# Kernel tuning notes

Hardware: AMD Instinct MI355X
Metric: run time of the kernel (lower is better)

Reference implementation:

```python
import jax, jax.numpy as jnp
import numpy as np


def setup_inputs() -> dict:
    key = jax.random.key(0)
    k1, k2, k3 = jax.random.split(key, 3)
    shape = (2, 16, 2048, 64)  # (b, num_heads, seq_len, d_k)
    Q = jax.random.normal(k1, shape, dtype=jnp.float32)
    K = jax.random.normal(k2, shape, dtype=jnp.float32)
    V = jax.random.normal(k3, shape, dtype=jnp.float32)
    return {"Q": Q, "K": K, "V": V}


def reference(Q, K, V):
    # Mathematically identical to the blockwise online-softmax loop:
    # causal softmax attention with scale 1/sqrt(d_k), plus logsumexp L.
    d_k = Q.shape[-1]
    seq_len = Q.shape[2]
    scale = 1.0 / np.sqrt(d_k).astype(np.float32)
    # scores: [b, h, q, k]
    S = jnp.einsum("bhqd,bhkd->bhqk", Q, K) * scale
    causal_mask = jnp.tril(jnp.ones((seq_len, seq_len), dtype=bool))  # k_pos <= q_pos
    S = jnp.where(causal_mask, S, -jnp.inf)
    # L_i = m_i + log(l_i) == logsumexp over key dim (every row has >=1 valid key)
    L = jax.nn.logsumexp(S, axis=-1, keepdims=True)  # [b, h, q, 1]
    P = jnp.exp(S - L)  # normalized probabilities (deferred-normalization result)
    O = jnp.einsum("bhqk,bhkd->bhqd", P, V)
    return O, L
```

## Files before the change

kernel.cpp:

```cpp
#include <hip/hip_runtime.h>
#include <hip/hip_bf16.h>

#define S_LEN 2048
#define DH    64
#define NBH   32
#define KSCALE 0.1803368801111f
#define LN2    0.6931471805599453f
#define MB2    4.0f

typedef short v4s __attribute__((ext_vector_type(4)));
typedef short v8s __attribute__((ext_vector_type(8)));
typedef float v4f __attribute__((ext_vector_type(4)));

__device__ __forceinline__ unsigned short f2bf(float f){
  union { float f; unsigned int u; } v; v.f = f;
  return (unsigned short)((v.u + 0x7FFFu + ((v.u >> 16) & 1u)) >> 16);
}

__device__ __forceinline__ void gld16(void* lds, const void* g){
  __builtin_amdgcn_global_load_lds(
      (const __attribute__((address_space(1))) unsigned int*)g,
      (__attribute__((address_space(3))) unsigned int*)lds, 16, 0, 0);
}

__global__ __launch_bounds__(256) void prep(const float* __restrict__ K,
                                            const float* __restrict__ V,
                                            unsigned short* __restrict__ Kf,
                                            unsigned short* __restrict__ Vf){
  __shared__ unsigned short s[64 * 72];
  const int t   = blockIdx.x;
  const int bh  = blockIdx.y;
  const int tid = threadIdx.x;

  const float* Ksrc = K + ((size_t)bh * S_LEN + t * 64) * DH;
  #pragma unroll
  for (int i = 0; i < 4; ++i){
    int f = tid + i * 256;
    float4 v = ((const float4*)Ksrc)[f];
    int row = f >> 4, col = (f & 15) * 4;
    ushort4 o; o.x = f2bf(v.x); o.y = f2bf(v.y); o.z = f2bf(v.z); o.w = f2bf(v.w);
    *(ushort4*)(&s[row * 72 + col]) = o;
  }
  __syncthreads();
  unsigned short* KfT = Kf + ((size_t)bh * 32 + t) * 4096;
  #pragma unroll
  for (int i = 0; i < 2; ++i){
    int item = tid + i * 256;
    int c = item >> 6, l = item & 63;
    int kb = c >> 1, h = c & 1;
    v8s frag = *(const v8s*)(&s[(kb * 16 + (l & 15)) * 72 + h * 32 + (l >> 4) * 8]);
    *(v8s*)(&KfT[c * 512 + l * 8]) = frag;
  }
  __syncthreads();

  const float* Vsrc = V + ((size_t)bh * S_LEN + t * 64) * DH;
  #pragma unroll
  for (int i = 0; i < 4; ++i){
    int f = tid + i * 256;
    float4 v = ((const float4*)Vsrc)[f];
    int k = f >> 4, d = (f & 15) * 4;
    s[(d + 0) * 72 + k] = f2bf(v.x);
    s[(d + 1) * 72 + k] = f2bf(v.y);
    s[(d + 2) * 72 + k] = f2bf(v.z);
    s[(d + 3) * 72 + k] = f2bf(v.w);
  }
  __syncthreads();
  unsigned short* VfT = Vf + ((size_t)bh * 32 + t) * 4096;
  #pragma unroll
  for (int i = 0; i < 2; ++i){
    int item = tid + i * 256;
    int c = item >> 6, l = item & 63;
    int kb = c >> 1, dp = c & 1;
    int kk = kb * 16 + (l >> 4) * 4;
    v4s a = *(const v4s*)(&s[((dp * 2 + 0) * 16 + (l & 15)) * 72 + kk]);
    v4s b = *(const v4s*)(&s[((dp * 2 + 1) * 16 + (l & 15)) * 72 + kk]);
    v8s fr; fr[0]=a[0]; fr[1]=a[1]; fr[2]=a[2]; fr[3]=a[3];
            fr[4]=b[0]; fr[5]=b[1]; fr[6]=b[2]; fr[7]=b[3];
    *(v8s*)(&VfT[c * 512 + l * 8]) = fr;
  }
}

__global__ __launch_bounds__(512, 4) void fa_fwd(
    const float* __restrict__ Q,
    const unsigned short* __restrict__ Kf,
    const unsigned short* __restrict__ Vf,
    float* __restrict__ O, float* __restrict__ L)
{
  __shared__ __align__(16) char smem[2][32768];

  const int tid  = threadIdx.x;
  const int w    = tid >> 6;
  const int lane = tid & 63;
  const int lq   = lane & 15;
  const int g    = lane >> 4;
  const int kq   = w >> 2;
  const int qs   = w & 3;
  const int bid  = blockIdx.x;
  const int o    = bid >> 5;
  const int r4   = o >> 3, a = o & 7;
  const int qt   = (r4 == 0) ? 31 - a : (r4 == 1) ? 16 + a
                 : (r4 == 2) ? 15 - a : a;
  const int bh   = bid & 31;
  const int M2   = (qt >> 1) + 1;
  const int qw0  = qt * 64 + qs * 16;

  const unsigned short* KfB = Kf + (size_t)bh * 32 * 4096;
  const unsigned short* VfB = Vf + (size_t)bh * 32 * 4096;

  auto issue = [&](int t, char* buf){
    const size_t base = (size_t)(2 * t) * 4096;
    gld16(buf +         tid * 16, KfB + base +        tid * 8);
    gld16(buf +  8192 + tid * 16, KfB + base + 4096 + tid * 8);
    gld16(buf + 16384 + tid * 16, VfB + base +        tid * 8);
    gld16(buf + 24576 + tid * 16, VfB + base + 4096 + tid * 8);
  };

  v8s qf[2];
  {
    const float* qp = Q + (size_t)(bh * S_LEN + qw0 + lq) * DH + g * 8;
    #pragma unroll
    for (int h = 0; h < 2; ++h){
      float4 aa = *(const float4*)(qp + h * 32);
      float4 bb = *(const float4*)(qp + h * 32 + 4);
      v8s qv;
      qv[0]=(short)f2bf(aa.x*KSCALE); qv[1]=(short)f2bf(aa.y*KSCALE);
      qv[2]=(short)f2bf(aa.z*KSCALE); qv[3]=(short)f2bf(aa.w*KSCALE);
      qv[4]=(short)f2bf(bb.x*KSCALE); qv[5]=(short)f2bf(bb.y*KSCALE);
      qv[6]=(short)f2bf(bb.z*KSCALE); qv[7]=(short)f2bf(bb.w*KSCALE);
      qf[h] = qv;
    }
  }

  issue(0, smem[0]);

  const v4f zero  = {0.f, 0.f, 0.f, 0.f};
  const v4f minit = {-MB2, -MB2, -MB2, -MB2};
  v4f acc[4];
  acc[0] = zero; acc[1] = zero; acc[2] = zero; acc[3] = zero;
  float l1 = 0.f;

  for (int t = 0; t < M2; ++t){
    const int tn = (t + 1 < M2) ? t + 1 : t;
    issue(tn, smem[(t + 1) & 1]);
    asm volatile("s_waitcnt vmcnt(4)" ::: "memory");
    __builtin_amdgcn_s_barrier();
    __builtin_amdgcn_sched_barrier(0);

    const int  kstart = t * 128 + kq * 64;
    const bool lastT  = (t + 1 == M2);
    const bool live   = !lastT || (kstart <= qw0 + 15);

    if (live){
      const char* kbase = smem[t & 1] +         kq * 8192;
      const char* vbase = smem[t & 1] + 16384 + kq * 8192;

      float p4[4][4];
      __builtin_amdgcn_s_setprio(1);
      #pragma unroll
      for (int j = 0; j < 4; ++j){
        v8s kf0 = *(const v8s*)(kbase + (j * 2    ) * 1024 + lane * 16);
        v8s kf1 = *(const v8s*)(kbase + (j * 2 + 1) * 1024 + lane * 16);
        v4f st = minit;
        st = __builtin_amdgcn_mfma_f32_16x16x32_bf16(kf0, qf[0], st, 0, 0, 0);
        st = __builtin_amdgcn_mfma_f32_16x16x32_bf16(kf1, qf[1], st, 0, 0, 0);
        p4[j][0] = st[0]; p4[j][1] = st[1]; p4[j][2] = st[2]; p4[j][3] = st[3];
      }
      __builtin_amdgcn_s_setprio(0);

      if (lastT){
        #pragma unroll
        for (int j = 0; j < 4; ++j)
          #pragma unroll
          for (int r = 0; r < 4; ++r)
            if (kstart + j * 16 + g * 4 + r > qw0 + lq) p4[j][r] = -INFINITY;
      }

      v4s pf[4];
      #pragma unroll
      for (int j = 0; j < 4; ++j){
        #pragma unroll
        for (int r = 0; r < 4; ++r){
          const float pe = __builtin_amdgcn_exp2f(p4[j][r]);
          p4[j][r] = pe;
          l1 += pe;
        }
        unsigned u0, u1;
        asm("v_cvt_pk_bf16_f32 %0, %1, %2" : "=v"(u0) : "v"(p4[j][0]), "v"(p4[j][1]));
        asm("v_cvt_pk_bf16_f32 %0, %1, %2" : "=v"(u1) : "v"(p4[j][2]), "v"(p4[j][3]));
        union { unsigned u[2]; v4s s4; } P; P.u[0] = u0; P.u[1] = u1;
        pf[j] = P.s4;
      }

      __builtin_amdgcn_s_setprio(1);
      #pragma unroll
      for (int j = 0; j < 4; ++j){
        #pragma unroll
        for (int dp = 0; dp < 2; ++dp){
          v8s vv8 = *(const v8s*)(vbase + (j * 2 + dp) * 1024 + lane * 16);
          v4s va0 = {vv8[0], vv8[1], vv8[2], vv8[3]};
          v4s va1 = {vv8[4], vv8[5], vv8[6], vv8[7]};
          acc[dp * 2    ] = __builtin_amdgcn_mfma_f32_16x16x16bf16_1k(va0, pf[j], acc[dp * 2    ], 0, 0, 0);
          acc[dp * 2 + 1] = __builtin_amdgcn_mfma_f32_16x16x16bf16_1k(va1, pf[j], acc[dp * 2 + 1], 0, 0, 0);
        }
      }
      __builtin_amdgcn_s_setprio(0);
    }
    __builtin_amdgcn_s_barrier();
    __builtin_amdgcn_sched_barrier(0);
  }

  asm volatile("s_waitcnt vmcnt(0)" ::: "memory");
  __builtin_amdgcn_sched_barrier(0);
  __syncthreads();

  l1 += __shfl_xor(l1, 16);
  l1 += __shfl_xor(l1, 32);

  float* Lx = (float*)(smem[1]);
  v4f*  Ox = (v4f*)(smem[0]);
  if (kq == 1){
    if (lane < 16) Lx[qs * 16 + lane] = l1;
    #pragma unroll
    for (int db = 0; db < 4; ++db)
      Ox[(qs * 4 + db) * 64 + lane] = acc[db];
  }
  __syncthreads();
  if (kq == 0){
    const float lt   = l1 + Lx[qs * 16 + lq];
    const float invl = 1.f / lt;
    float* Ob = O + ((size_t)bh * S_LEN + qw0 + lq) * DH;
    #pragma unroll
    for (int db = 0; db < 4; ++db){
      v4f o2 = (acc[db] + Ox[(qs * 4 + db) * 64 + lane]) * invl;
      *(v4f*)(Ob + db * 16 + g * 4) = o2;
    }
    if (lane < 16)
      L[(size_t)bh * S_LEN + qw0 + lane] = logf(lt) + MB2 * LN2;
  }
}

__global__ __launch_bounds__(64) void fa_naive(
    const float* __restrict__ Q, const float* __restrict__ K,
    const float* __restrict__ V, float* __restrict__ O, float* __restrict__ L)
{
  const int q  = blockIdx.x;
  const int bh = blockIdx.y;
  const int d  = threadIdx.x;
  const float qv = Q[(size_t)(bh * S_LEN + q) * DH + d];
  float m = -INFINITY, l = 0.f, o = 0.f;
  for (int k = 0; k <= q; ++k){
    float s = qv * K[(size_t)(bh * S_LEN + k) * DH + d];
    #pragma unroll
    for (int off = 32; off > 0; off >>= 1) s += __shfl_xor(s, off);
    s *= 0.125f;
    const float mn = fmaxf(m, s);
    const float sfc = expf(m - mn);
    const float pe = expf(s - mn);
    l = l * sfc + pe;
    o = o * sfc + pe * V[(size_t)(bh * S_LEN + k) * DH + d];
    m = mn;
  }
  O[(size_t)(bh * S_LEN + q) * DH + d] = o / l;
  if (d == 0) L[(size_t)bh * S_LEN + q] = m + logf(l);
}

extern "C" void kernel_launch(void* const* d_in, const int* in_sizes, int n_in,
                              void* d_out, int out_size, void* d_ws, size_t ws_size,
                              hipStream_t stream)
{
  (void)in_sizes; (void)n_in; (void)out_size;
  const float* Q = (const float*)d_in[0];
  const float* K = (const float*)d_in[1];
  const float* V = (const float*)d_in[2];
  float* O = (float*)d_out;
  float* L = O + (size_t)NBH * S_LEN * DH;

  const size_t half = (size_t)NBH * S_LEN * DH * sizeof(unsigned short);
  if (ws_size >= 2 * half){
    unsigned short* Kf = (unsigned short*)d_ws;
    unsigned short* Vf = Kf + (size_t)NBH * S_LEN * DH;
    prep<<<dim3(S_LEN / 64, NBH), 256, 0, stream>>>(K, V, Kf, Vf);
    fa_fwd<<<dim3(1024), 512, 0, stream>>>(Q, Kf, Vf, O, L);
  } else {
    fa_naive<<<dim3(S_LEN, NBH), 64, 0, stream>>>(Q, K, V, O, L);
  }
}
```

Baseline: 44.00 us.

## Switch to 64-key tiles with triple-buffered LDS and split-key waves

Each loop step now covers 64 keys instead of 128, with the two key-quarter wave groups each handling 32 keys of the tile. A three-buffer LDS ring prefetches two tiles ahead, and the shared-memory footprint shrinks from 64KB to 48KB. The launch bound is raised to 6 blocks per CU, trading more loop iterations and barriers for finer causal skipping, deeper prefetch and potentially higher occupancy. All K/V fragments are loaded up front and the QK MFMAs are interleaved.

```diff
diff --git a/kernel.cpp b/kernel.cpp
--- a/kernel.cpp
+++ b/kernel.cpp
@@ -80,13 +80,13 @@
   }
 }
 
-__global__ __launch_bounds__(512, 4) void fa_fwd(
+__global__ __launch_bounds__(512, 6) void fa_fwd(
     const float* __restrict__ Q,
     const unsigned short* __restrict__ Kf,
     const unsigned short* __restrict__ Vf,
     float* __restrict__ O, float* __restrict__ L)
 {
-  __shared__ __align__(16) char smem[2][32768];
+  __shared__ __align__(16) char smem[3][16384];
 
   const int tid  = threadIdx.x;
   const int w    = tid >> 6;
@@ -101,18 +101,15 @@
   const int qt   = (r4 == 0) ? 31 - a : (r4 == 1) ? 16 + a
                  : (r4 == 2) ? 15 - a : a;
   const int bh   = bid & 31;
-  const int M2   = (qt >> 1) + 1;
+  const int M    = qt + 1;
   const int qw0  = qt * 64 + qs * 16;
 
   const unsigned short* KfB = Kf + (size_t)bh * 32 * 4096;
   const unsigned short* VfB = Vf + (size_t)bh * 32 * 4096;
 
   auto issue = [&](int t, char* buf){
-    const size_t base = (size_t)(2 * t) * 4096;
-    gld16(buf +         tid * 16, KfB + base +        tid * 8);
-    gld16(buf +  8192 + tid * 16, KfB + base + 4096 + tid * 8);
-    gld16(buf + 16384 + tid * 16, VfB + base +        tid * 8);
-    gld16(buf + 24576 + tid * 16, VfB + base + 4096 + tid * 8);
+    gld16(buf +        tid * 16, KfB + (size_t)t * 4096 + tid * 8);
+    gld16(buf + 8192 + tid * 16, VfB + (size_t)t * 4096 + tid * 8);
   };
 
   v8s qf[2];
@@ -132,6 +129,7 @@
   }
 
   issue(0, smem[0]);
+  issue((1 <= qt) ? 1 : 1, smem[1]);
 
   const v4f zero  = {0.f, 0.f, 0.f, 0.f};
   const v4f minit = {-MB2, -MB2, -MB2, -MB2};
@@ -139,45 +137,58 @@
   acc[0] = zero; acc[1] = zero; acc[2] = zero; acc[3] = zero;
   float l1 = 0.f;
 
-  for (int t = 0; t < M2; ++t){
-    const int tn = (t + 1 < M2) ? t + 1 : t;
-    issue(tn, smem[(t + 1) & 1]);
+  const bool diagLive = (kq * 32 <= qs * 16 + 15);
+
+  int bcur = 0;
+  for (int t = 0; t < M; ++t){
+    int tn2 = t + 2; if (tn2 > 31) tn2 = 31;
+    int b2 = bcur + 2; if (b2 >= 3) b2 -= 3;
+    issue(tn2, smem[b2]);
     asm volatile("s_waitcnt vmcnt(4)" ::: "memory");
     __builtin_amdgcn_s_barrier();
     __builtin_amdgcn_sched_barrier(0);
 
-    const int  kstart = t * 128 + kq * 64;
-    const bool lastT  = (t + 1 == M2);
-    const bool live   = !lastT || (kstart <= qw0 + 15);
-
-    if (live){
-      const char* kbase = smem[t & 1] +         kq * 8192;
-      const char* vbase = smem[t & 1] + 16384 + kq * 8192;
-
-      float p4[4][4];
+    if (t < qt || diagLive){
+      const char* kbase = smem[bcur];
+      const char* vbase = smem[bcur] + 8192;
+
+      const int koff0 = (kq * 4    ) * 1024 + lane * 16;
+      const int koff1 = (kq * 4 + 1) * 1024 + lane * 16;
+      const int koff2 = (kq * 4 + 2) * 1024 + lane * 16;
+      const int koff3 = (kq * 4 + 3) * 1024 + lane * 16;
+      v8s kf0 = *(const v8s*)(kbase + koff0);
+      v8s kf1 = *(const v8s*)(kbase + koff1);
+      v8s kf2 = *(const v8s*)(kbase + koff2);
+      v8s kf3 = *(const v8s*)(kbase + koff3);
+      v8s vv0 = *(const v8s*)(vbase + koff0);
+      v8s vv1 = *(const v8s*)(vbase + koff1);
+      v8s vv2 = *(const v8s*)(vbase + koff2);
+      v8s vv3 = *(const v8s*)(vbase + koff3);
+
+      float p4[2][4];
       __builtin_amdgcn_s_setprio(1);
-      #pragma unroll
-      for (int j = 0; j < 4; ++j){
-        v8s kf0 = *(const v8s*)(kbase + (j * 2    ) * 1024 + lane * 16);
-        v8s kf1 = *(const v8s*)(kbase + (j * 2 + 1) * 1024 + lane * 16);
-        v4f st = minit;
-        st = __builtin_amdgcn_mfma_f32_16x16x32_bf16(kf0, qf[0], st, 0, 0, 0);
-        st = __builtin_amdgcn_mfma_f32_16x16x32_bf16(kf1, qf[1], st, 0, 0, 0);
-        p4[j][0] = st[0]; p4[j][1] = st[1]; p4[j][2] = st[2]; p4[j][3] = st[3];
+      {
+        v4f st0 = minit, st1 = minit;
+        st0 = __builtin_amdgcn_mfma_f32_16x16x32_bf16(kf0, qf[0], st0, 0, 0, 0);
+        st1 = __builtin_amdgcn_mfma_f32_16x16x32_bf16(kf2, qf[0], st1, 0, 0, 0);
+        st0 = __builtin_amdgcn_mfma_f32_16x16x32_bf16(kf1, qf[1], st0, 0, 0, 0);
+        st1 = __builtin_amdgcn_mfma_f32_16x16x32_bf16(kf3, qf[1], st1, 0, 0, 0);
+        #pragma unroll
+        for (int r = 0; r < 4; ++r){ p4[0][r] = st0[r]; p4[1][r] = st1[r]; }
       }
       __builtin_amdgcn_s_setprio(0);
 
-      if (lastT){
+      if (t == qt){
         #pragma unroll
-        for (int j = 0; j < 4; ++j)
+        for (int j = 0; j < 2; ++j)
           #pragma unroll
           for (int r = 0; r < 4; ++r)
-            if (kstart + j * 16 + g * 4 + r > qw0 + lq) p4[j][r] = -INFINITY;
+            if (kq * 32 + j * 16 + g * 4 + r > qs * 16 + lq) p4[j][r] = -INFINITY;
       }
 
-      v4s pf[4];
+      v4s pf[2];
       #pragma unroll
-      for (int j = 0; j < 4; ++j){
+      for (int j = 0; j < 2; ++j){
         #pragma unroll
         for (int r = 0; r < 4; ++r){
           const float pe = __builtin_amdgcn_exp2f(p4[j][r]);
@@ -192,21 +203,29 @@
       }
 
       __builtin_amdgcn_s_setprio(1);
-      #pragma unroll
-      for (int j = 0; j < 4; ++j){
-        #pragma unroll
-        for (int dp = 0; dp < 2; ++dp){
-          v8s vv8 = *(const v8s*)(vbase + (j * 2 + dp) * 1024 + lane * 16);
-          v4s va0 = {vv8[0], vv8[1], vv8[2], vv8[3]};
-          v4s va1 = {vv8[4], vv8[5], vv8[6], vv8[7]};
-          acc[dp * 2    ] = __builtin_amdgcn_mfma_f32_16x16x16bf16_1k(va0, pf[j], acc[dp * 2    ], 0, 0, 0);
-          acc[dp * 2 + 1] = __builtin_amdgcn_mfma_f32_16x16x16bf16_1k(va1, pf[j], acc[dp * 2 + 1], 0, 0, 0);
-        }
+      {
+        v4s va0 = {vv0[0], vv0[1], vv0[2], vv0[3]};
+        v4s va1 = {vv0[4], vv0[5], vv0[6], vv0[7]};
+        v4s vb0 = {vv1[0], vv1[1], vv1[2], vv1[3]};
+        v4s vb1 = {vv1[4], vv1[5], vv1[6], vv1[7]};
+        acc[0] = __builtin_amdgcn_mfma_f32_16x16x16bf16_1k(va0, pf[0], acc[0], 0, 0, 0);
+        acc[1] = __builtin_amdgcn_mfma_f32_16x16x16bf16_1k(va1, pf[0], acc[1], 0, 0, 0);
+        acc[2] = __builtin_amdgcn_mfma_f32_16x16x16bf16_1k(vb0, pf[0], acc[2], 0, 0, 0);
+        acc[3] = __builtin_amdgcn_mfma_f32_16x16x16bf16_1k(vb1, pf[0], acc[3], 0, 0, 0);
+        v4s vc0 = {vv2[0], vv2[1], vv2[2], vv2[3]};
+        v4s vc1 = {vv2[4], vv2[5], vv2[6], vv2[7]};
+        v4s vd0 = {vv3[0], vv3[1], vv3[2], vv3[3]};
+        v4s vd1 = {vv3[4], vv3[5], vv3[6], vv3[7]};
+        acc[0] = __builtin_amdgcn_mfma_f32_16x16x16bf16_1k(vc0, pf[1], acc[0], 0, 0, 0);
+        acc[1] = __builtin_amdgcn_mfma_f32_16x16x16bf16_1k(vc1, pf[1], acc[1], 0, 0, 0);
+        acc[2] = __builtin_amdgcn_mfma_f32_16x16x16bf16_1k(vd0, pf[1], acc[2], 0, 0, 0);
+        acc[3] = __builtin_amdgcn_mfma_f32_16x16x16bf16_1k(vd1, pf[1], acc[3], 0, 0, 0);
       }
       __builtin_amdgcn_s_setprio(0);
     }
     __builtin_amdgcn_s_barrier();
     __builtin_amdgcn_sched_barrier(0);
+    ++bcur; if (bcur == 3) bcur = 0;
   }
 
   asm volatile("s_waitcnt vmcnt(0)" ::: "memory");
```

Measured after the change: 42.68 us. 1.03x faster.
